# Kernel tuning notes

Hardware: AMD Instinct MI355X
Metric: run time of the kernel (lower is better)

## Reference

```python
import jax, jax.numpy as jnp
import numpy as np

B, N, T, L = 4, 512, 288, 128
NEG_SLOPE = 0.2
TEMPERATURE = 0.2
CLAMP = 10.0
EPS = 1e-10


def setup_inputs() -> dict:
    key = jax.random.key(0)
    ks = jax.random.split(key, 6)
    s_in = 1.0 / np.sqrt(T)
    s_lat = 1.0 / np.sqrt(2 * L)
    s_b = 1.0 / np.sqrt(L)
    x = jax.random.normal(ks[0], (B, N, T), dtype=jnp.float32)
    W1 = jax.random.normal(ks[1], (L, T), dtype=jnp.float32) * s_in
    W2 = jax.random.normal(ks[2], (L, T), dtype=jnp.float32) * s_in
    Wp = jax.random.normal(ks[3], (L, 2 * L), dtype=jnp.float32) * s_lat
    Wb = jax.random.normal(ks[4], (L,), dtype=jnp.float32) * s_b
    noise = jnp.clip(jax.random.uniform(ks[5], (N, N), dtype=jnp.float32), 1e-6, 1.0 - 1e-6)
    return {
        "x": x,
        "W1": W1, "b1": jnp.zeros((L,), jnp.float32),
        "W2": W2, "b2": jnp.zeros((L,), jnp.float32),
        "Wp": Wp, "bp": jnp.zeros((L,), jnp.float32),
        "Wb": Wb, "bb": jnp.zeros((1,), jnp.float32),
        "noise": noise,
    }


def _leaky(v):
    return jnp.where(v >= 0, v, NEG_SLOPE * v)


def reference(x, W1, b1, W2, b2, Wp, bp, Wb, bb, noise):
    # per-node projections (B, N, L)
    x1 = _leaky(jnp.einsum('bnt,lt->bnl', x, W1) + b1)
    x2 = _leaky(jnp.einsum('bnt,lt->bnl', x, W2) + b2)
    # linear_para_latent(cat(x1_i, x2_j)) == x1_i @ Wp_a^T + x2_j @ Wp_b^T + bp
    Wp_a, Wp_b = Wp[:, :L], Wp[:, L:]
    s1 = jnp.einsum('bnl,ml->bnm', x1, Wp_a)  # (B, N, L_out)
    s2 = jnp.einsum('bnl,ml->bnm', x2, Wp_b)
    pair = s1[:, :, None, :] + s2[:, None, :, :] + bp  # (B, N, N, L)
    h = _leaky(pair)
    logits = jnp.einsum('bijl,l->bij', h, Wb) + bb[0]  # (B, N, N)
    p = jax.nn.sigmoid(logits).mean(axis=0)            # (N, N)
    p = p * (1.0 - jnp.eye(N, dtype=p.dtype))          # fill_diagonal_(0)
    # relaxed Bernoulli sample (binary concrete) with logit clamping
    logit_p = jnp.clip(jnp.log(p + EPS) - jnp.log1p(-p + EPS), -CLAMP, CLAMP)
    logistic = jnp.log(noise) - jnp.log1p(-noise)
    adj = jax.nn.sigmoid((logit_p + logistic) / TEMPERATURE)
    return adj
```

## Files before the change

kernel.cpp:

```cpp
#include <hip/hip_runtime.h>
#include <hip/hip_bf16.h>
#include <math.h>

#define NN 512
#define NT 288

__global__ __launch_bounds__(256) void kT(
    const float* __restrict__ W1, const float* __restrict__ W2,
    const float* __restrict__ Wp,
    float* __restrict__ Wt, float* __restrict__ Wpt)
{
    int g = blockIdx.x * 256 + threadIdx.x;
    if (g < 288 * 256) {
        int k = g >> 8, col = g & 255;
        Wt[g] = (col < 128) ? W1[col * 288 + k] : W2[(col - 128) * 288 + k];
    } else {
        int h = g - 288 * 256;
        int k = h >> 8, col = h & 255;
        Wpt[h] = (col < 128) ? Wp[col * 256 + k]
                             : Wp[(col - 128) * 256 + 128 + k];
    }
}

__global__ __launch_bounds__(512) void kP(
    const float* __restrict__ x,
    const float* __restrict__ Wt,
    const float* __restrict__ b1,
    const float* __restrict__ b2,
    const float* __restrict__ Wpt,
    const float* __restrict__ bp,
    const float* __restrict__ Wb,
    const float* __restrict__ bb,
    float* __restrict__ S12,
    float* __restrict__ Aarr,
    float* __restrict__ Carr)
{
    __shared__ __align__(16) float xs[8 * NT];
    __shared__ __align__(16) float x12s[8 * 256];
    __shared__ __align__(16) float ph[7 * 2048];
    __shared__ __align__(16) float s12s[8 * 260];

    const int t   = threadIdx.x;
    const int bn0 = blockIdx.x * 8;
    const int c4  = t & 63;
    const int khe = t >> 6;

    for (int q = 0; q < 2; ++q) {
        int idx = q * 512 + t;
        if (idx < 576) {
            int row = idx / 72, cc = idx % 72;
            *(float4*)&xs[row * NT + cc * 4] =
                *(const float4*)&x[(size_t)(bn0 + row) * NT + cc * 4];
        }
    }
    __syncthreads();

    float acc[8][4];
#pragma unroll
    for (int n = 0; n < 8; ++n)
#pragma unroll
        for (int c = 0; c < 4; ++c) acc[n][c] = 0.0f;

    const int kbase1 = khe * 36;
#pragma unroll 2
    for (int k4 = 0; k4 < 9; ++k4) {
        const int k0 = kbase1 + k4 * 4;
        float4 w0 = *(const float4*)&Wt[(size_t)(k0 + 0) * 256 + c4 * 4];
        float4 w1 = *(const float4*)&Wt[(size_t)(k0 + 1) * 256 + c4 * 4];
        float4 w2 = *(const float4*)&Wt[(size_t)(k0 + 2) * 256 + c4 * 4];
        float4 w3 = *(const float4*)&Wt[(size_t)(k0 + 3) * 256 + c4 * 4];
        const float* w0p = (const float*)&w0;
        const float* w1p = (const float*)&w1;
        const float* w2p = (const float*)&w2;
        const float* w3p = (const float*)&w3;
#pragma unroll
        for (int n = 0; n < 8; ++n) {
            float4 xv = *(const float4*)&xs[n * NT + k0];
#pragma unroll
            for (int c = 0; c < 4; ++c) {
                acc[n][c] = fmaf(xv.x, w0p[c], acc[n][c]);
                acc[n][c] = fmaf(xv.y, w1p[c], acc[n][c]);
                acc[n][c] = fmaf(xv.z, w2p[c], acc[n][c]);
                acc[n][c] = fmaf(xv.w, w3p[c], acc[n][c]);
            }
        }
    }

    if (khe) {
#pragma unroll
        for (int n = 0; n < 8; ++n) {
            float4 v = {acc[n][0], acc[n][1], acc[n][2], acc[n][3]};
            *(float4*)&ph[(khe - 1) * 2048 + n * 256 + c4 * 4] = v;
        }
    }
    __syncthreads();
    if (!khe) {
        float4 bias4 = (c4 < 32) ? *(const float4*)&b1[c4 * 4]
                                 : *(const float4*)&b2[(c4 - 32) * 4];
        const float* bp4 = (const float*)&bias4;
#pragma unroll
        for (int n = 0; n < 8; ++n) {
            float s0 = acc[n][0], s1 = acc[n][1], s2 = acc[n][2], s3 = acc[n][3];
#pragma unroll
            for (int p = 0; p < 7; ++p) {
                float4 v = *(const float4*)&ph[p * 2048 + n * 256 + c4 * 4];
                s0 += v.x; s1 += v.y; s2 += v.z; s3 += v.w;
            }
            float4 r;
            float* rp = (float*)&r;
            float sv[4] = {s0, s1, s2, s3};
#pragma unroll
            for (int c = 0; c < 4; ++c) {
                float v = sv[c] + bp4[c];
                rp[c] = fmaxf(v, 0.2f * v);
            }
            *(float4*)&x12s[n * 256 + c4 * 4] = r;
        }
    }
    __syncthreads();

    float acc2[8][4];
#pragma unroll
    for (int n = 0; n < 8; ++n)
#pragma unroll
        for (int c = 0; c < 4; ++c) acc2[n][c] = 0.0f;

    const int koff = (c4 < 32) ? 0 : 128;
    const int kbase2 = khe * 16;
#pragma unroll 2
    for (int k4 = 0; k4 < 4; ++k4) {
        const int k0 = kbase2 + k4 * 4;
        float4 w0 = *(const float4*)&Wpt[(size_t)(k0 + 0) * 256 + c4 * 4];
        float4 w1 = *(const float4*)&Wpt[(size_t)(k0 + 1) * 256 + c4 * 4];
        float4 w2 = *(const float4*)&Wpt[(size_t)(k0 + 2) * 256 + c4 * 4];
        float4 w3 = *(const float4*)&Wpt[(size_t)(k0 + 3) * 256 + c4 * 4];
        const float* w0p = (const float*)&w0;
        const float* w1p = (const float*)&w1;
        const float* w2p = (const float*)&w2;
        const float* w3p = (const float*)&w3;
#pragma unroll
        for (int n = 0; n < 8; ++n) {
            float4 xv = *(const float4*)&x12s[n * 256 + koff + k0];
#pragma unroll
            for (int c = 0; c < 4; ++c) {
                acc2[n][c] = fmaf(xv.x, w0p[c], acc2[n][c]);
                acc2[n][c] = fmaf(xv.y, w1p[c], acc2[n][c]);
                acc2[n][c] = fmaf(xv.z, w2p[c], acc2[n][c]);
                acc2[n][c] = fmaf(xv.w, w3p[c], acc2[n][c]);
            }
        }
    }

    if (khe) {
#pragma unroll
        for (int n = 0; n < 8; ++n) {
            float4 v = {acc2[n][0], acc2[n][1], acc2[n][2], acc2[n][3]};
            *(float4*)&ph[(khe - 1) * 2048 + n * 256 + c4 * 4] = v;
        }
    }
    __syncthreads();
    if (!khe) {
        float4 bias4;
        if (c4 < 32) bias4 = *(const float4*)&bp[c4 * 4];
        else         bias4 = make_float4(0.f, 0.f, 0.f, 0.f);
        const float* bp4 = (const float*)&bias4;
#pragma unroll
        for (int n = 0; n < 8; ++n) {
            float s0 = acc2[n][0], s1 = acc2[n][1], s2 = acc2[n][2], s3 = acc2[n][3];
#pragma unroll
            for (int p = 0; p < 7; ++p) {
                float4 v = *(const float4*)&ph[p * 2048 + n * 256 + c4 * 4];
                s0 += v.x; s1 += v.y; s2 += v.z; s3 += v.w;
            }
            float sv[4] = {s0, s1, s2, s3};
            float4 r;
            float* rp = (float*)&r;
#pragma unroll
            for (int c = 0; c < 4; ++c) rp[c] = sv[c] + bp4[c];
            *(float4*)&S12[(size_t)(bn0 + n) * 256 + c4 * 4] = r;
            *(float4*)&s12s[n * 260 + c4 * 4] = r;
        }
    }
    __syncthreads();

    {
        int lane32 = t & 31;
        int n = (t >> 5) & 7;
        int isC = t >> 8;
        int base = isC ? 128 : 0;
        float sum = 0.0f;
#pragma unroll
        for (int s = 0; s < 4; ++s) {
            int j = lane32 + s * 32;
            sum = fmaf(s12s[n * 260 + base + j], Wb[j], sum);
        }
#pragma unroll
        for (int m = 16; m >= 1; m >>= 1)
            sum += __shfl_xor(sum, m, 32);
        if (lane32 == 0) {
            if (isC) Carr[bn0 + n] = 0.6f * sum;
            else     Aarr[bn0 + n] = 0.6f * sum + bb[0];
        }
    }
}

__global__ __launch_bounds__(512) void kQ(
    const float* __restrict__ S12,
    const float* __restrict__ Aarr,
    const float* __restrict__ Carr,
    const float* __restrict__ Wb,
    const float* __restrict__ noise,
    float* __restrict__ out)
{
    __shared__ __align__(16) float smem[32768];
    float* S1t = smem;
    float* S2t = smem + 16384;

    const int t = threadIdx.x;
    const int bx = blockIdx.x, by = blockIdx.y;

#pragma unroll
    for (int q = 0; q < 16; ++q) {
        int task = q * 512 + t;
        int isS2 = task >> 12;
        int r    = task & 4095;
        int bz   = r >> 10;
        int row  = (r >> 5) & 31;
        int c4   = r & 31;
        size_t src = (size_t)(bz * NN + (isS2 ? by : bx) * 32 + row) * 256
                     + (isS2 ? 128 : 0) + c4 * 4;
        float4 v = *(const float4*)&S12[src];
        float* dst = (isS2 ? S2t : S1t) + bz * 4096;
        int rw = row ^ ((c4 & 7) << 2);
        dst[(c4 * 4 + 0) * 32 + rw] = v.x;
        dst[(c4 * 4 + 1) * 32 + rw] = v.y;
        dst[(c4 * 4 + 2) * 32 + rw] = v.z;
        dst[(c4 * 4 + 3) * 32 + rw] = v.w;
    }
    __syncthreads();

    const int lh = t >> 8;
    const int bz = (t >> 6) & 3;
    const int s  = t & 63;
    const int i0 = (s >> 3) << 2, j0 = (s & 7) << 2;

    const float* S1b = S1t + bz * 4096 + lh * 64 * 32;
    const float* S2b = S2t + bz * 4096 + lh * 64 * 32;
    const float* wbp = Wb + lh * 64;

    float accv[16];
#pragma unroll
    for (int k = 0; k < 16; ++k) accv[k] = 0.0f;

    for (int l4 = 0; l4 < 16; ++l4) {
        const int sw = (l4 & 7) << 2;
        const int lrow = l4 * 4 * 32;
        float4 wv = *(const float4*)&wbp[l4 * 4];
        const float wl[4] = {wv.x, wv.y, wv.z, wv.w};
#pragma unroll
        for (int d = 0; d < 4; ++d) {
            float4 a = *(const float4*)&S1b[lrow + d * 32 + (i0 ^ sw)];
            float4 b = *(const float4*)&S2b[lrow + d * 32 + (j0 ^ sw)];
            float w = wl[d];
            float ai[4] = {a.x, a.y, a.z, a.w};
            float bj[4] = {b.x, b.y, b.z, b.w};
#pragma unroll
            for (int ii = 0; ii < 4; ++ii)
#pragma unroll
                for (int jj = 0; jj < 4; ++jj) {
                    float tv = ai[ii] + bj[jj];
                    accv[ii * 4 + jj] = fmaf(fabsf(tv), w, accv[ii * 4 + jj]);
                }
        }
    }

    float* red = smem;
    const int tid2 = t & 255;
    __syncthreads();
    if (lh) {
#pragma unroll
        for (int q = 0; q < 4; ++q) {
            float4 v = {accv[4 * q], accv[4 * q + 1], accv[4 * q + 2], accv[4 * q + 3]};
            *(float4*)&red[q * 1024 + tid2 * 4] = v;
        }
    }
    __syncthreads();

    float sig[16];
    if (!lh) {
#pragma unroll
        for (int q = 0; q < 4; ++q) {
            float4 v = *(const float4*)&red[q * 1024 + tid2 * 4];
            accv[4 * q]     += v.x;
            accv[4 * q + 1] += v.y;
            accv[4 * q + 2] += v.z;
            accv[4 * q + 3] += v.w;
        }
        float Av[4], Cv[4];
#pragma unroll
        for (int ii = 0; ii < 4; ++ii) Av[ii] = Aarr[bz * NN + bx * 32 + i0 + ii];
#pragma unroll
        for (int jj = 0; jj < 4; ++jj) Cv[jj] = Carr[bz * NN + by * 32 + j0 + jj];
#pragma unroll
        for (int ii = 0; ii < 4; ++ii)
#pragma unroll
            for (int jj = 0; jj < 4; ++jj) {
                float lg = Av[ii] + Cv[jj] + 0.4f * accv[ii * 4 + jj];
                sig[ii * 4 + jj] = 1.0f / (1.0f + expf(-lg));
            }
        float* redB = smem + 4096;
        if (bz) {
#pragma unroll
            for (int q = 0; q < 4; ++q) {
                float4 v = {sig[4 * q], sig[4 * q + 1], sig[4 * q + 2], sig[4 * q + 3]};
                *(float4*)&redB[(bz - 1) * 1024 + q * 256 + s * 4] = v;
            }
        }
    }
    __syncthreads();

    float* redB = smem + 4096;
    float* redP = smem + 7168;
    if (t < 64) {
#pragma unroll
        for (int bzz = 0; bzz < 3; ++bzz)
#pragma unroll
            for (int q = 0; q < 4; ++q) {
                float4 v = *(const float4*)&redB[bzz * 1024 + q * 256 + t * 4];
                sig[4 * q]     += v.x;
                sig[4 * q + 1] += v.y;
                sig[4 * q + 2] += v.z;
                sig[4 * q + 3] += v.w;
            }
#pragma unroll
        for (int q = 0; q < 4; ++q) {
            float4 v = {sig[4 * q], sig[4 * q + 1], sig[4 * q + 2], sig[4 * q + 3]};
            *(float4*)&redP[t * 16 + q * 4] = v;
        }
    }
    __syncthreads();

    if (t < 256) {
        int i   = t >> 3;
        int j0f = (t & 7) * 4;
        int sP  = (t >> 5) * 8 + (t & 7);
        int k0  = ((t >> 3) & 3) * 4;
        float4 pv4 = *(const float4*)&redP[sP * 16 + k0];
        float pv[4] = {pv4.x, pv4.y, pv4.z, pv4.w};

        int gi = bx * 32 + i;
        size_t base = (size_t)gi * NN + by * 32 + j0f;
        float4 nz = *(const float4*)&noise[base];
        float nv[4] = {nz.x, nz.y, nz.z, nz.w};

        float4 o;
        float* op = (float*)&o;
#pragma unroll
        for (int c = 0; c < 4; ++c) {
            float p = 0.25f * pv[c];
            int gj = by * 32 + j0f + c;
            if (gj == gi) p = 0.0f;
            float lp = logf(p + 1e-10f) - log1pf(-p + 1e-10f);
            lp = fminf(fmaxf(lp, -10.0f), 10.0f);
            float lgs = logf(nv[c]) - log1pf(-nv[c]);
            op[c] = 1.0f / (1.0f + expf(-(lp + lgs) * 5.0f));
        }
        *(float4*)&out[base] = o;
    }
}

extern "C" void kernel_launch(void* const* d_in, const int* in_sizes, int n_in,
                              void* d_out, int out_size, void* d_ws, size_t ws_size,
                              hipStream_t stream) {
    const float* x     = (const float*)d_in[0];
    const float* W1    = (const float*)d_in[1];
    const float* b1    = (const float*)d_in[2];
    const float* W2    = (const float*)d_in[3];
    const float* b2    = (const float*)d_in[4];
    const float* Wp    = (const float*)d_in[5];
    const float* bp    = (const float*)d_in[6];
    const float* Wb    = (const float*)d_in[7];
    const float* bb    = (const float*)d_in[8];
    const float* noise = (const float*)d_in[9];

    float* ws   = (float*)d_ws;
    float* S12  = ws;
    float* Aarr = ws + 524288;
    float* Carr = Aarr + 2048;
    float* Wt   = Carr + 2048;
    float* Wpt  = Wt + 73728;

    kT<<<416, 256, 0, stream>>>(W1, W2, Wp, Wt, Wpt);
    kP<<<256, 512, 0, stream>>>(x, Wt, b1, b2, Wpt, bp, Wb, bb,
                                S12, Aarr, Carr);
    kQ<<<dim3(16, 16), 512, 0, stream>>>(S12, Aarr, Carr, Wb, noise,
                                         (float*)d_out);
}
```

Baseline: 38.29 us.

## Use 8x4 register tiles with four-way latent split in pairwise kernel

Changes the per-thread tile in the pairwise logit kernel from 4x4 to 8x4 outputs and splits the latent dimension across four thread groups of 32 latents instead of two groups of 64. Each S2 load is now reused across eight rows, which cuts LDS reads per FMA. The cost is twice the accumulator registers, a three-way cross-group shared-memory reduction, and a larger smem footprint. Only 128 threads now do the sigmoid stage and 32 threads do the batch reduction.

```diff
diff --git a/kernel.cpp b/kernel.cpp
--- a/kernel.cpp
+++ b/kernel.cpp
@@ -239,33 +239,38 @@
     }
     __syncthreads();
 
-    const int lh = t >> 8;
-    const int bz = (t >> 6) & 3;
-    const int s  = t & 63;
-    const int i0 = (s >> 3) << 2, j0 = (s & 7) << 2;
-
-    const float* S1b = S1t + bz * 4096 + lh * 64 * 32;
-    const float* S2b = S2t + bz * 4096 + lh * 64 * 32;
-    const float* wbp = Wb + lh * 64;
-
-    float accv[16];
-#pragma unroll
-    for (int k = 0; k < 16; ++k) accv[k] = 0.0f;
-
-    for (int l4 = 0; l4 < 16; ++l4) {
-        const int sw = (l4 & 7) << 2;
-        const int lrow = l4 * 4 * 32;
+    const int lq = t >> 7;
+    const int bz = (t >> 5) & 3;
+    const int s  = t & 31;
+    const int i0 = (s >> 3) * 8;
+    const int j0 = (s & 7) * 4;
+
+    const float* S1b = S1t + bz * 4096 + lq * 1024;
+    const float* S2b = S2t + bz * 4096 + lq * 1024;
+    const float* wbp = Wb + lq * 32;
+
+    float accv[32];
+#pragma unroll
+    for (int k = 0; k < 32; ++k) accv[k] = 0.0f;
+
+    for (int l4 = 0; l4 < 8; ++l4) {
+        const int sw = l4 << 2;
+        const int lrow = l4 * 128;
+        const int ia = i0 ^ sw;
+        const int ib = (i0 + 4) ^ sw;
+        const int jb = j0 ^ sw;
         float4 wv = *(const float4*)&wbp[l4 * 4];
         const float wl[4] = {wv.x, wv.y, wv.z, wv.w};
 #pragma unroll
         for (int d = 0; d < 4; ++d) {
-            float4 a = *(const float4*)&S1b[lrow + d * 32 + (i0 ^ sw)];
-            float4 b = *(const float4*)&S2b[lrow + d * 32 + (j0 ^ sw)];
+            float4 a0 = *(const float4*)&S1b[lrow + d * 32 + ia];
+            float4 a1 = *(const float4*)&S1b[lrow + d * 32 + ib];
+            float4 b0 = *(const float4*)&S2b[lrow + d * 32 + jb];
             float w = wl[d];
-            float ai[4] = {a.x, a.y, a.z, a.w};
-            float bj[4] = {b.x, b.y, b.z, b.w};
-#pragma unroll
-            for (int ii = 0; ii < 4; ++ii)
+            float ai[8] = {a0.x, a0.y, a0.z, a0.w, a1.x, a1.y, a1.z, a1.w};
+            float bj[4] = {b0.x, b0.y, b0.z, b0.w};
+#pragma unroll
+            for (int ii = 0; ii < 8; ++ii)
 #pragma unroll
                 for (int jj = 0; jj < 4; ++jj) {
                     float tv = ai[ii] + bj[jj];
@@ -275,67 +280,75 @@
     }
 
     float* red = smem;
-    const int tid2 = t & 255;
-    __syncthreads();
-    if (lh) {
-#pragma unroll
-        for (int q = 0; q < 4; ++q) {
-            float4 v = {accv[4 * q], accv[4 * q + 1], accv[4 * q + 2], accv[4 * q + 3]};
-            *(float4*)&red[q * 1024 + tid2 * 4] = v;
-        }
-    }
-    __syncthreads();
-
-    float sig[16];
-    if (!lh) {
-#pragma unroll
-        for (int q = 0; q < 4; ++q) {
-            float4 v = *(const float4*)&red[q * 1024 + tid2 * 4];
-            accv[4 * q]     += v.x;
-            accv[4 * q + 1] += v.y;
-            accv[4 * q + 2] += v.z;
-            accv[4 * q + 3] += v.w;
-        }
-        float Av[4], Cv[4];
-#pragma unroll
-        for (int ii = 0; ii < 4; ++ii) Av[ii] = Aarr[bz * NN + bx * 32 + i0 + ii];
-#pragma unroll
-        for (int jj = 0; jj < 4; ++jj) Cv[jj] = Carr[bz * NN + by * 32 + j0 + jj];
-#pragma unroll
-        for (int ii = 0; ii < 4; ++ii)
+    const int tid2 = t & 127;
+    __syncthreads();
+    if (lq) {
+#pragma unroll
+        for (int q = 0; q < 8; ++q) {
+            float4 v = {accv[4 * q], accv[4 * q + 1],
+                        accv[4 * q + 2], accv[4 * q + 3]};
+            *(float4*)&red[(lq - 1) * 4096 + q * 512 + tid2 * 4] = v;
+        }
+    }
+    __syncthreads();
+
+    float sig[32];
+    float* redB = smem + 12288;
+    if (!lq) {
+#pragma unroll
+        for (int p = 0; p < 3; ++p)
+#pragma unroll
+            for (int q = 0; q < 8; ++q) {
+                float4 v = *(const float4*)&red[p * 4096 + q * 512 + tid2 * 4];
+                accv[4 * q]     += v.x;
+                accv[4 * q + 1] += v.y;
+                accv[4 * q + 2] += v.z;
+                accv[4 * q + 3] += v.w;
+            }
+        float Av[8], Cv[4];
+        {
+            float4 av0 = *(const float4*)&Aarr[bz * NN + bx * 32 + i0];
+            float4 av1 = *(const float4*)&Aarr[bz * NN + bx * 32 + i0 + 4];
+            Av[0]=av0.x; Av[1]=av0.y; Av[2]=av0.z; Av[3]=av0.w;
+            Av[4]=av1.x; Av[5]=av1.y; Av[6]=av1.z; Av[7]=av1.w;
+            float4 cv = *(const float4*)&Carr[bz * NN + by * 32 + j0];
+            Cv[0]=cv.x; Cv[1]=cv.y; Cv[2]=cv.z; Cv[3]=cv.w;
+        }
+#pragma unroll
+        for (int ii = 0; ii < 8; ++ii)
 #pragma unroll
             for (int jj = 0; jj < 4; ++jj) {
                 float lg = Av[ii] + Cv[jj] + 0.4f * accv[ii * 4 + jj];
                 sig[ii * 4 + jj] = 1.0f / (1.0f + expf(-lg));
             }
-        float* redB = smem + 4096;
         if (bz) {
 #pragma unroll
-            for (int q = 0; q < 4; ++q) {
-                float4 v = {sig[4 * q], sig[4 * q + 1], sig[4 * q + 2], sig[4 * q + 3]};
-                *(float4*)&redB[(bz - 1) * 1024 + q * 256 + s * 4] = v;
-            }
-        }
-    }
-    __syncthreads();
-
-    float* redB = smem + 4096;
-    float* redP = smem + 7168;
-    if (t < 64) {
+            for (int q = 0; q < 8; ++q) {
+                float4 v = {sig[4 * q], sig[4 * q + 1],
+                            sig[4 * q + 2], sig[4 * q + 3]};
+                *(float4*)&redB[(bz - 1) * 1024 + q * 128 + s * 4] = v;
+            }
+        }
+    }
+    __syncthreads();
+
+    float* redP = smem + 15360;
+    if (t < 32) {
 #pragma unroll
         for (int bzz = 0; bzz < 3; ++bzz)
 #pragma unroll
-            for (int q = 0; q < 4; ++q) {
-                float4 v = *(const float4*)&redB[bzz * 1024 + q * 256 + t * 4];
+            for (int q = 0; q < 8; ++q) {
+                float4 v = *(const float4*)&redB[bzz * 1024 + q * 128 + t * 4];
                 sig[4 * q]     += v.x;
                 sig[4 * q + 1] += v.y;
                 sig[4 * q + 2] += v.z;
                 sig[4 * q + 3] += v.w;
             }
 #pragma unroll
-        for (int q = 0; q < 4; ++q) {
-            float4 v = {sig[4 * q], sig[4 * q + 1], sig[4 * q + 2], sig[4 * q + 3]};
-            *(float4*)&redP[t * 16 + q * 4] = v;
+        for (int q = 0; q < 8; ++q) {
+            float4 v = {sig[4 * q], sig[4 * q + 1],
+                        sig[4 * q + 2], sig[4 * q + 3]};
+            *(float4*)&redP[q * 128 + t * 4] = v;
         }
     }
     __syncthreads();
@@ -343,9 +356,9 @@
     if (t < 256) {
         int i   = t >> 3;
         int j0f = (t & 7) * 4;
-        int sP  = (t >> 5) * 8 + (t & 7);
-        int k0  = ((t >> 3) & 3) * 4;
-        float4 pv4 = *(const float4*)&redP[sP * 16 + k0];
+        int ii  = i & 7;
+        int sP  = (i >> 3) * 8 + (t & 7);
+        float4 pv4 = *(const float4*)&redP[ii * 128 + sP * 4];
         float pv[4] = {pv4.x, pv4.y, pv4.z, pv4.w};
 
         int gi = bx * 32 + i;
```

Measured after the change: 39.00 us. Within noise of the previous version (+1.8%).
